# Performance work log

Measured on AMD Instinct MI355X. Metric: run time of the kernel, lower is better.

Reference implementation:

```python
import jax, jax.numpy as jnp
import numpy as np

B, L, HS = 32, 128, 512
P, M = 12, 1024
V, D = 50000, 128
P_TOTAL = 16
CHAR_LEN, CHAR_V = 16, 100
PRI_POS = (0, 1, 2, 3)  # privacy POS tags
TEMP = 1.0              # eval-mode temperature


def setup_inputs() -> dict:
    key = jax.random.key(0)
    ks = jax.random.split(key, 16)
    return {
        "ctx": jax.random.normal(ks[0], (B, L, HS), jnp.float32),
        "dec_W": jax.random.normal(ks[1], (P, HS, M), jnp.float32) * 0.05,
        "dec_b": jax.random.normal(ks[2], (P, M), jnp.float32) * 0.05,
        "psr_weight": jax.random.normal(ks[3], (V, D), jnp.float32),
        "atk_weight": jax.random.normal(ks[4], (V, D), jnp.float32),
        "cpy_W1": jax.random.normal(ks[5], (HS, 64), jnp.float32) * 0.05,
        "cpy_b1": jax.random.normal(ks[6], (64,), jnp.float32) * 0.05,
        "cpy_W2": jax.random.normal(ks[7], (64, 2), jnp.float32) * 0.05,
        "cpy_b2": jax.random.normal(ks[8], (2,), jnp.float32) * 0.05,
        "inp_word": jax.random.randint(ks[9], (B, L), 0, V),
        "inp_pos": jax.random.randint(ks[10], (B, L), 0, P_TOTAL),
        "inp_mask": jnp.ones((B, L), jnp.int32),
        "words": jax.random.randint(ks[11], (P, M), 0, V),
        "lut": jax.random.randint(ks[12], (V, CHAR_LEN), 0, CHAR_V),
    }


def _gumbel_softmax_hard(logits, key, t):
    # hard (straight-through) gumbel-softmax; forward value is one-hot
    u = jax.random.uniform(key, logits.shape, logits.dtype, 1e-6, 1.0 - 1e-6)
    g = -jnp.log(-jnp.log(u))
    y = jax.nn.softmax((logits + g) / t, axis=-1)
    idx = jnp.argmax(y, axis=-1)
    y_hard = jax.nn.one_hot(idx, logits.shape[-1], dtype=y.dtype)
    return y_hard + y - jax.lax.stop_gradient(y), idx


def reference(ctx, dec_W, dec_b, psr_weight, atk_weight,
              cpy_W1, cpy_b1, cpy_W2, cpy_b2,
              inp_word, inp_pos, inp_mask, words, lut):
    bs, ls = inp_word.shape
    N = bs * ls
    gkey = jax.random.key(42)

    ctx_f = ctx.reshape(N, -1)                      # [N, HS]
    pos_f = inp_pos.reshape(N)
    word_f = inp_word.reshape(N)

    ori_psr = psr_weight[word_f]                    # [N, D] gather
    ori_atk = atk_weight[word_f]
    obf_word = word_f
    obf_psr = ori_psr
    obf_atk = ori_atk
    obf_mask = jnp.zeros((N,), bool)
    pri_mask = jnp.zeros((N,), bool)
    entropy = jnp.float32(0.0)

    for p in range(P):  # small fixed set of POS tags (structurally distinct decoders)
        m = pos_f == p                              # [N] routing mask
        obf_mask = obf_mask | m
        if p in PRI_POS:
            pri_mask = pri_mask | m
        cnt = jnp.sum(m.astype(jnp.int32))
        logp = jax.nn.log_softmax(ctx_f @ dec_W[p] + dec_b[p], axis=-1)  # [N, M]
        ent_elem = -logp * jnp.exp(logp)
        ent_p = jnp.sum(jnp.where(m[:, None], ent_elem, 0.0)) / jnp.maximum(cnt * M, 1).astype(jnp.float32)
        entropy = entropy + jnp.where(cnt > 0, ent_p, 0.0)
        spt, idx = _gumbel_softmax_hard(logp, jax.random.fold_in(gkey, p), TEMP)
        spt_word = words[p][idx]                    # map local id -> vocab id
        obf_word = jnp.where(m, spt_word, obf_word)
        psr_p = spt @ psr_weight[words[p]]          # [N, D], per-POS sub-table
        atk_p = spt @ atk_weight[words[p]]
        obf_psr = jnp.where(m[:, None], psr_p, obf_psr)
        obf_atk = jnp.where(m[:, None], atk_p, obf_atk)

    # copy classifier
    h = jax.nn.relu(ctx_f @ cpy_W1 + cpy_b1)
    pcpy = jax.nn.log_softmax(h @ cpy_W2 + cpy_b2, axis=-1)  # [N, 2]
    # do_not_copy_pri: force pcpy to [0, 1] on privacy tokens
    pcpy = jnp.where(pri_mask[:, None], jnp.array([0.0, 1.0], pcpy.dtype), pcpy)

    cpy, _ = _gumbel_softmax_hard(pcpy, jax.random.fold_in(gkey, 999), TEMP)  # [N, 2]
    mask_f = inp_mask.reshape(N).astype(bool)
    cpy_mask = (cpy[:, 0] == 1.0) & mask_f

    noroot = inp_mask.astype(bool).at[:, 0].set(False).reshape(N)
    nr_cnt = jnp.maximum(jnp.sum(noroot.astype(jnp.int32)), 1).astype(jnp.float32)
    logp2 = jax.nn.log_softmax(pcpy, axis=-1)       # F.cross_entropy applies log_softmax again
    cpy_loss = -jnp.sum(jnp.where(noroot, logp2[:, 1], 0.0)) / nr_cnt  # cpy_penalty = 1.0 (applied twice)

    # use_copy: blend original vs obfuscated via (hard) copy gate
    c0, c1 = cpy[:, 0:1], cpy[:, 1:2]
    psr_out = (ori_psr * c0 + obf_psr * c1).reshape(bs, ls, -1)
    atk_out = (ori_atk * c0 + obf_atk * c1).reshape(bs, ls, -1)
    obf_mask = obf_mask & ~cpy_mask
    out_word = (word_f.astype(jnp.float32) * cpy[:, 0]
                + obf_word.astype(jnp.float32) * cpy[:, 1]).astype(jnp.int32).reshape(bs, ls)

    obf_char = lut[out_word]                        # [B, L, CHAR_LEN]
    ent_loss = -entropy  # ent_penalty = 1.0

    return (out_word, obf_char, psr_out, atk_out,
            obf_mask.reshape(bs, ls), cpy_mask.reshape(bs, ls),
            pri_mask.reshape(bs, ls), cpy_loss, ent_loss)
```

## Files before the change

### kernel.cpp

```cpp
#include <hip/hip_runtime.h>
#include <math.h>

#define BB 32
#define LL 128
#define HSZ 512
#define PP 12
#define MM 1024
#define VV 50000
#define DD 128
#define CLEN 16
#define NTOT 4096
#define LISTCAP 512

#define RT 64
#define CT 64
#define BK2 32
#define CPB 16

#define OFF_WORD  0
#define OFF_CHAR  4096
#define OFF_PSR   69632
#define OFF_ATK   593920
#define OFF_OBFM  1118208
#define OFF_CPYM  1122304
#define OFF_PRIM  1126400
#define OFF_CLOSS 1130496
#define OFF_ELOSS 1130497

#define WS_SC_OFF     6656
#define WS_LOGITS_OFF 16384

__device__ __forceinline__ float EXP32(float x){ return (float)exp((double)x); }
__device__ __forceinline__ float LOG32(float x){ return (float)log((double)x); }

__device__ __forceinline__ unsigned rotl32(unsigned x, int r){ return (x<<r)|(x>>(32-r)); }
__device__ __forceinline__ void tf2x32(unsigned k0, unsigned k1, unsigned x0, unsigned x1,
                                       unsigned &o0, unsigned &o1){
  unsigned ks2 = k0 ^ k1 ^ 0x1BD11BDAu;
  x0 += k0; x1 += k1;
  x0+=x1; x1=rotl32(x1,13); x1^=x0;
  x0+=x1; x1=rotl32(x1,15); x1^=x0;
  x0+=x1; x1=rotl32(x1,26); x1^=x0;
  x0+=x1; x1=rotl32(x1, 6); x1^=x0;
  x0+=k1; x1+=ks2+1u;
  x0+=x1; x1=rotl32(x1,17); x1^=x0;
  x0+=x1; x1=rotl32(x1,29); x1^=x0;
  x0+=x1; x1=rotl32(x1,16); x1^=x0;
  x0+=x1; x1=rotl32(x1,24); x1^=x0;
  x0+=ks2; x1+=k0+2u;
  x0+=x1; x1=rotl32(x1,13); x1^=x0;
  x0+=x1; x1=rotl32(x1,15); x1^=x0;
  x0+=x1; x1=rotl32(x1,26); x1^=x0;
  x0+=x1; x1=rotl32(x1, 6); x1^=x0;
  x0+=k0; x1+=k1+3u;
  x0+=x1; x1=rotl32(x1,17); x1^=x0;
  x0+=x1; x1=rotl32(x1,29); x1^=x0;
  x0+=x1; x1=rotl32(x1,16); x1^=x0;
  x0+=x1; x1=rotl32(x1,24); x1^=x0;
  x0+=k1; x1+=ks2+4u;
  x0+=x1; x1=rotl32(x1,13); x1^=x0;
  x0+=x1; x1=rotl32(x1,15); x1^=x0;
  x0+=x1; x1=rotl32(x1,26); x1^=x0;
  x0+=x1; x1=rotl32(x1, 6); x1^=x0;
  x0+=ks2; x1+=k0+5u;
  o0=x0; o1=x1;
}

__device__ __forceinline__ unsigned tf_bits32(unsigned k0, unsigned k1, unsigned e){
  unsigned o0, o1; tf2x32(k0, k1, 0u, e, o0, o1); return o0 ^ o1;
}

__device__ __forceinline__ float bits_to_unif(unsigned bits){
  const float lo = 1e-6f;
  const float hi = (float)(1.0 - 1e-6);
  const float span = hi - lo;
  unsigned fb = (bits >> 9) | 0x3f800000u;
  float f = __fsub_rn(__uint_as_float(fb), 1.0f);
  float r = __fadd_rn(__fmul_rn(f, span), lo);
  return fmaxf(lo, r);
}

__device__ __forceinline__ float gumbel_exact(unsigned bits){
  float u = bits_to_unif(bits);
  float v = -LOG32(u);
  return -LOG32(v);
}
__device__ __forceinline__ float gumbel_fast(unsigned bits){
  float u = bits_to_unif(bits);
  float v = -logf(u);
  return -logf(v);
}

__device__ __forceinline__ void gate_chain(int n, int pos,
                                           float p0f, float p1f,
                                           const float* __restrict__ cb2,
                                           float* __restrict__ sc_enc,
                                           float* __restrict__ l21_out)
{
  const bool ispri = (pos < 4);
  float pc0 = __fadd_rn(p0f, cb2[0]);
  float pc1 = __fadd_rn(p1f, cb2[1]);
  float m2  = fmaxf(pc0, pc1);
  float s0  = __fsub_rn(pc0, m2), s1 = __fsub_rn(pc1, m2);
  float se  = __fadd_rn(EXP32(s0), EXP32(s1));
  float lse = LOG32(se);
  float q0  = __fsub_rn(s0, lse), q1 = __fsub_rn(s1, lse);
  if (ispri){ q0 = 0.0f; q1 = 1.0f; }

  unsigned k90, k91; tf2x32(0u, 42u, 0u, 999u, k90, k91);
  float g0 = gumbel_exact(tf_bits32(k90, k91, (unsigned)(2*n)));
  float g1 = gumbel_exact(tf_bits32(k90, k91, (unsigned)(2*n + 1)));

  float x0 = __fadd_rn(q0, g0), x1 = __fadd_rn(q1, g1);
  float mmv = fmaxf(x0, x1);
  float ex0 = EXP32(__fsub_rn(x0, mmv));
  float ex1 = EXP32(__fsub_rn(x1, mmv));
  float ssum = __fadd_rn(ex0, ex1);
  float y0 = __fdiv_rn(ex0, ssum), y1 = __fdiv_rn(ex1, ssum);
  int   idx2 = (y1 > y0) ? 1 : 0;
  float ysel = idx2 ? y1 : y0;
  float c    = __fsub_rn(__fadd_rn(1.0f, ysel), ysel);
  *sc_enc = idx2 ? c : -c;

  float m3 = fmaxf(q0, q1);
  float t0 = __fsub_rn(q0, m3), t1 = __fsub_rn(q1, m3);
  float se2 = __fadd_rn(EXP32(t0), EXP32(t1));
  *l21_out = __fsub_rn(t1, LOG32(se2));
}

__global__ __launch_bounds__(256)
void bucket_kernel(const int* __restrict__ inp_pos, int* __restrict__ cntg,
                   int* __restrict__ rowlist)
{
  const int p = blockIdx.x;
  const int t = threadIdx.x;
  const int w = t >> 6, lane = t & 63;
  __shared__ int wtot[4];
  __shared__ int base_s;
  if (t == 0) base_s = 0;
  __syncthreads();
  for (int n0 = 0; n0 < NTOT; n0 += 256){
    int n = n0 + t;
    int m = (inp_pos[n] == p) ? 1 : 0;
    unsigned long long bal = __ballot(m);
    int excl = __popcll(bal & ((1ULL << lane) - 1ULL));
    if (lane == 0) wtot[w] = __popcll(bal);
    __syncthreads();
    int wbase = 0;
    #pragma unroll
    for (int i = 0; i < 4; ++i) if (i < w) wbase += wtot[i];
    int tot = wtot[0] + wtot[1] + wtot[2] + wtot[3];
    int b = base_s;
    if (m){
      int slot = b + wbase + excl;
      if (slot < LISTCAP) rowlist[p*LISTCAP + slot] = n;
    }
    __syncthreads();
    if (t == 0) base_s = b + tot;
    __syncthreads();
  }
  if (t == 0) cntg[p] = base_s;
}

__global__ __launch_bounds__(256)
void cpy_build_kernel(const float* __restrict__ ctx, const float* __restrict__ cW1,
                      const float* __restrict__ cb1, const float* __restrict__ cW2,
                      const float* __restrict__ cb2, const int* __restrict__ inp_pos,
                      float* __restrict__ scbuf)
{
  const int n0 = blockIdx.x * CPB;
  const int t = threadIdx.x;

  __shared__ float W1s[64][68];
  __shared__ float Cs[CPB][68];

  const int r  = t >> 4;
  const int og = (t & 15) * 4;
  double acc[4] = {0.0, 0.0, 0.0, 0.0};

  for (int k0 = 0; k0 < HSZ; k0 += 64){
    #pragma unroll
    for (int i = 0; i < 4; ++i){
      int s = t + i*256;
      int kk = s >> 4, q = s & 15;
      float4 v = *(const float4*)(cW1 + (size_t)(k0+kk)*64 + q*4);
      *(float4*)&W1s[kk][q*4] = v;
    }
    {
      int rr = t >> 4, q = t & 15;
      float4 v = *(const float4*)(ctx + (size_t)(n0+rr)*HSZ + k0 + q*4);
      *(float4*)&Cs[rr][q*4] = v;
    }
    __syncthreads();
    #pragma unroll 4
    for (int kk = 0; kk < 64; ++kk){
      double c = (double)Cs[r][kk];
      acc[0] += c * (double)W1s[kk][og+0];
      acc[1] += c * (double)W1s[kk][og+1];
      acc[2] += c * (double)W1s[kk][og+2];
      acc[3] += c * (double)W1s[kk][og+3];
    }
    __syncthreads();
  }

  double p0 = 0.0, p1 = 0.0;
  #pragma unroll
  for (int j = 0; j < 4; ++j){
    float hv = __fadd_rn((float)acc[j], cb1[og+j]);
    hv = hv > 0.f ? hv : 0.f;
    double hd = (double)hv;
    p0 += hd * (double)cW2[2*(og+j)+0];
    p1 += hd * (double)cW2[2*(og+j)+1];
  }
  #pragma unroll
  for (int off = 1; off < 16; off <<= 1){
    p0 += __shfl_xor(p0, off);
    p1 += __shfl_xor(p1, off);
  }

  if ((t & 15) == 0){
    const int n = n0 + r;
    float senc, l21;
    gate_chain(n, inp_pos[n], (float)p0, (float)p1, cb2, &senc, &l21);
    scbuf[2*n + 0] = senc;
    scbuf[2*n + 1] = l21;
  }
}

__global__ __launch_bounds__(256)
void gemm_kernel(const float* __restrict__ ctx, const float* __restrict__ dec_W,
                 const int* __restrict__ cntg, const int* __restrict__ rowlist,
                 float* __restrict__ logits)
{
  const int p  = blockIdx.z;
  const int c0 = blockIdx.x * CT;
  const int r0 = blockIdx.y * RT;
  const int cnt0 = cntg[p];
  const int cnt  = cnt0 < LISTCAP ? cnt0 : LISTCAP;
  if (r0 >= cnt) return;
  const int t = threadIdx.x;

  __shared__ double As[RT][BK2+2];
  __shared__ double Bs[BK2][16][6];
  __shared__ int    rid_s[RT];

  if (t < RT){
    int rr = r0 + t;
    rid_s[t] = rowlist[p*LISTCAP + (rr < cnt ? rr : cnt-1)];
  }
  __syncthreads();

  const int tr = t >> 4, tc = t & 15;
  double acc[4][4];
  #pragma unroll
  for (int i = 0; i < 4; ++i)
    #pragma unroll
    for (int j = 0; j < 4; ++j) acc[i][j] = 0.0;

  const float* Wp = dec_W + (size_t)p * HSZ * MM;

  for (int k0 = 0; k0 < HSZ; k0 += BK2){
    #pragma unroll
    for (int i = 0; i < 2; ++i){
      int s = t + i*256;
      int rr = s >> 3, q = s & 7;
      float4 v = *(const float4*)(ctx + (size_t)rid_s[rr]*HSZ + k0 + q*4);
      double2 d0; d0.x = (double)v.x; d0.y = (double)v.y;
      double2 d1; d1.x = (double)v.z; d1.y = (double)v.w;
      *(double2*)&As[rr][q*4 + 0] = d0;
      *(double2*)&As[rr][q*4 + 2] = d1;
    }
    #pragma unroll
    for (int i = 0; i < 2; ++i){
      int s = t + i*256;
      int kk = s >> 4, q = s & 15;
      float4 v = *(const float4*)(Wp + (size_t)(k0+kk)*MM + c0 + q*4);
      double2 d0; d0.x = (double)v.x; d0.y = (double)v.y;
      double2 d1; d1.x = (double)v.z; d1.y = (double)v.w;
      *(double2*)&Bs[kk][q][0] = d0;
      *(double2*)&Bs[kk][q][2] = d1;
    }
    __syncthreads();
    #pragma unroll 4
    for (int kk = 0; kk < BK2; ++kk){
      double b0 = Bs[kk][tc][0];
      double b1 = Bs[kk][tc][1];
      double b2 = Bs[kk][tc][2];
      double b3 = Bs[kk][tc][3];
      double a0 = As[tr*4+0][kk];
      double a1 = As[tr*4+1][kk];
      double a2 = As[tr*4+2][kk];
      double a3 = As[tr*4+3][kk];
      acc[0][0]+=a0*b0; acc[0][1]+=a0*b1; acc[0][2]+=a0*b2; acc[0][3]+=a0*b3;
      acc[1][0]+=a1*b0; acc[1][1]+=a1*b1; acc[1][2]+=a1*b2; acc[1][3]+=a1*b3;
      acc[2][0]+=a2*b0; acc[2][1]+=a2*b1; acc[2][2]+=a2*b2; acc[2][3]+=a2*b3;
      acc[3][0]+=a3*b0; acc[3][1]+=a3*b1; acc[3][2]+=a3*b2; acc[3][3]+=a3*b3;
    }
    __syncthreads();
  }

  #pragma unroll
  for (int i = 0; i < 4; ++i){
    int rr = r0 + tr*4 + i;
    if (rr < cnt){
      int rg = rid_s[tr*4 + i];
      float4 o;
      o.x=(float)acc[i][0]; o.y=(float)acc[i][1]; o.z=(float)acc[i][2]; o.w=(float)acc[i][3];
      *(float4*)(logits + (size_t)rg*MM + c0 + tc*4) = o;
    }
  }
}

__global__ __launch_bounds__(256)
void finalize_kernel(const float* __restrict__ dec_b,
                     const float* __restrict__ psr_w, const float* __restrict__ atk_w,
                     const int* __restrict__ inp_word, const int* __restrict__ inp_pos,
                     const int* __restrict__ inp_mask, const int* __restrict__ words,
                     const int* __restrict__ lut, float* __restrict__ logitsbuf,
                     const float* __restrict__ scbuf,
                     float* __restrict__ out)
{
  const int wid = threadIdx.x >> 6, lane = threadIdx.x & 63;
  const int n = blockIdx.x * 4 + wid;

  const int  pos   = inp_pos[n];
  const int  word  = inp_word[n];
  const int  msk   = inp_mask[n];
  const bool isobf = (pos < PP);
  const bool ispri = (pos < 4);
  const float senc = scbuf[2*n + 0];
  const float c0 = (senc < 0.f) ? -senc : 0.f;
  const float c1 = (senc < 0.f) ? 0.f : senc;

  int bi = 0;
  if (isobf){
    float l[16];
    float lm = -3.4e38f;
    #pragma unroll
    for (int it = 0; it < 4; ++it){
      int m = it*256 + lane*4;
      float4 lg = *(const float4*)(logitsbuf + (size_t)n*MM + m);
      float4 bq = *(const float4*)(dec_b + (size_t)pos*MM + m);
      l[it*4+0] = __fadd_rn(lg.x, bq.x);
      l[it*4+1] = __fadd_rn(lg.y, bq.y);
      l[it*4+2] = __fadd_rn(lg.z, bq.z);
      l[it*4+3] = __fadd_rn(lg.w, bq.w);
      lm = fmaxf(lm, fmaxf(fmaxf(l[it*4+0], l[it*4+1]), fmaxf(l[it*4+2], l[it*4+3])));
    }
    #pragma unroll
    for (int off = 32; off > 0; off >>= 1) lm = fmaxf(lm, __shfl_xor(lm, off));
    const float xmax = lm;

    float e[16];
    double ds = 0.0;
    #pragma unroll
    for (int j = 0; j < 16; ++j){
      e[j] = expf(__fsub_rn(l[j], xmax));
      ds += (double)e[j];
    }
    #pragma unroll
    for (int off = 32; off > 0; off >>= 1) ds += __shfl_xor(ds, off);
    const double se = ds;
    const float lse = logf((float)se);
    const double inv_se = 1.0 / se;

    unsigned kp0, kp1; tf2x32(0u, 42u, 0u, (unsigned)pos, kp0, kp1);
    float best = -3.4e38f; double es = 0.0;
    #pragma unroll
    for (int it = 0; it < 4; ++it){
      #pragma unroll
      for (int j = 0; j < 4; ++j){
        int m = it*256 + lane*4 + j;
        float sh = __fsub_rn(l[it*4+j], xmax);
        float lp = __fsub_rn(sh, lse);
        es += (double)(-lp) * ((double)e[it*4+j] * inv_se);
        float g = gumbel_fast(tf_bits32(kp0, kp1, (unsigned)(n*MM + m)));
        float sv = __fadd_rn(lp, g);
        if (sv > best){ best = sv; bi = m; }
      }
    }
    #pragma unroll
    for (int off = 32; off > 0; off >>= 1){
      float ov = __shfl_xor(best, off);
      int   oi = __shfl_xor(bi,   off);
      if (ov > best || (ov == best && oi < bi)){ best = ov; bi = oi; }
      es += __shfl_xor(es, off);
    }
    if (lane == 0) logitsbuf[(size_t)n*MM] = (float)es;
  } else {
    if (lane == 0) logitsbuf[(size_t)n*MM] = 0.f;
  }

  const int obf_word = isobf ? words[pos*MM + bi] : word;
  float of = __fadd_rn(__fmul_rn((float)word, c0), __fmul_rn((float)obf_word, c1));
  int ow = (int)of;
  if (lane == 0){
    out[OFF_WORD + n] = (float)ow;
    bool cpym = (c0 == 1.0f) && (msk != 0);
    out[OFF_CPYM + n] = cpym ? 1.f : 0.f;
    out[OFF_OBFM + n] = (isobf && !cpym) ? 1.f : 0.f;
    out[OFF_PRIM + n] = ispri ? 1.f : 0.f;
  }
  if (lane < CLEN)
    out[OFF_CHAR + (size_t)n*CLEN + lane] = (float)lut[(size_t)ow*CLEN + lane];
  #pragma unroll
  for (int rep = 0; rep < 2; ++rep){
    int j = lane + rep*64;
    float po = psr_w[(size_t)word*DD + j];
    float pb = isobf ? psr_w[(size_t)obf_word*DD + j] : po;
    out[OFF_PSR + (size_t)n*DD + j] = __fadd_rn(__fmul_rn(po, c0), __fmul_rn(pb, c1));
    float ao = atk_w[(size_t)word*DD + j];
    float ab = isobf ? atk_w[(size_t)obf_word*DD + j] : ao;
    out[OFF_ATK + (size_t)n*DD + j] = __fadd_rn(__fmul_rn(ao, c0), __fmul_rn(ab, c1));
  }
}

__global__ __launch_bounds__(1024)
void fin2_kernel(const int* __restrict__ inp_pos, const int* __restrict__ inp_mask,
                 const float* __restrict__ scbuf, const float* __restrict__ logitsbuf,
                 float* __restrict__ out)
{
  const int t = threadIdx.x;
  const int w = t >> 6, lane = t & 63;
  __shared__ double s_ent[PP];
  __shared__ int    s_cnt[PP];
  __shared__ double s_cl;
  __shared__ int    s_nr;

  if (w < PP){
    const int p = w;
    double es = 0.0; int c = 0;
    for (int n = lane; n < NTOT; n += 64){
      if (inp_pos[n] == p){
        es += (double)logitsbuf[(size_t)n*MM];
        c  += 1;
      }
    }
    #pragma unroll
    for (int off = 1; off < 64; off <<= 1){
      es += __shfl_xor(es, off);
      c  += __shfl_xor(c, off);
    }
    if (lane == 0){ s_ent[p] = es; s_cnt[p] = c; }
  } else if (w == PP){
    double cl = 0.0; int nr = 0;
    for (int n = lane; n < NTOT; n += 64){
      if (inp_mask[n] != 0 && (n & (LL-1)) != 0){
        cl += (double)scbuf[2*n + 1];
        nr += 1;
      }
    }
    #pragma unroll
    for (int off = 1; off < 64; off <<= 1){
      cl += __shfl_xor(cl, off);
      nr += __shfl_xor(nr, off);
    }
    if (lane == 0){ s_cl = cl; s_nr = nr; }
  }
  __syncthreads();
  if (t == 0){
    float ent = 0.f;
    for (int p = 0; p < PP; ++p){
      int c = s_cnt[p];
      if (c > 0){
        int denom = c * MM; if (denom < 1) denom = 1;
        ent = __fadd_rn(ent, __fdiv_rn((float)s_ent[p], (float)denom));
      }
    }
    out[OFF_ELOSS] = -ent;
    int nrc = s_nr; if (nrc < 1) nrc = 1;
    out[OFF_CLOSS] = -__fdiv_rn((float)s_cl, (float)nrc);
  }
}

__global__ __launch_bounds__(256)
void fin_kernel(const int* __restrict__ inp_pos, const int* __restrict__ inp_mask,
                const float* __restrict__ ws, float* __restrict__ out)
{
  __shared__ int cnt[PP];
  __shared__ int nr;
  int t = threadIdx.x;
  if (t < PP) cnt[t] = 0;
  if (t == 0) nr = 0;
  __syncthreads();
  int ln = 0;
  for (int n = t; n < NTOT; n += 256){
    int p = inp_pos[n];
    if (p < PP) atomicAdd(&cnt[p], 1);
    if (inp_mask[n] != 0 && (n & (LL-1)) != 0) ln++;
  }
  atomicAdd(&nr, ln);
  __syncthreads();
  if (t == 0){
    float ent = 0.f;
    for (int p = 0; p < PP; ++p){
      int c = cnt[p];
      if (c > 0){
        int denom = c * MM; if (denom < 1) denom = 1;
        ent = __fadd_rn(ent, __fdiv_rn(ws[p], (float)denom));
      }
    }
    out[OFF_ELOSS] = -ent;
    int nrc = nr; if (nrc < 1) nrc = 1;
    out[OFF_CLOSS] = -__fdiv_rn(ws[12], (float)nrc);
  }
}

__global__ __launch_bounds__(256)
void row_kernel_mono(const float* __restrict__ ctx, const float* __restrict__ dec_W,
                const float* __restrict__ dec_b, const float* __restrict__ psr_w,
                const float* __restrict__ atk_w, const float* __restrict__ cW1,
                const float* __restrict__ cb1, const float* __restrict__ cW2,
                const float* __restrict__ cb2, const int* __restrict__ inp_word,
                const int* __restrict__ inp_pos, const int* __restrict__ inp_mask,
                const int* __restrict__ words, const int* __restrict__ lut,
                float* __restrict__ out, float* __restrict__ ws)
{
  const int n = blockIdx.x;
  const int t = threadIdx.x;

  __shared__ float  ctx_s[HSZ];
  __shared__ float  logit_s[MM];
  __shared__ float  h_s[64];
  __shared__ double redd[256];
  __shared__ float  redf[256];
  __shared__ int    redi[256];
  __shared__ float  sc[2];
  __shared__ int    si[1];

  for (int k = t; k < HSZ; k += 256) ctx_s[k] = ctx[(size_t)n*HSZ + k];
  __syncthreads();

  const int  pos   = inp_pos[n];
  const int  word  = inp_word[n];
  const int  msk   = inp_mask[n];
  const bool isobf = (pos < PP);
  const bool ispri = (pos < 4);

  if (t < 64){
    double acc = 0.0;
    for (int k = 0; k < HSZ; ++k) acc += (double)ctx_s[k] * (double)cW1[k*64 + t];
    float hv = __fadd_rn((float)acc, cb1[t]);
    h_s[t] = hv > 0.f ? hv : 0.f;
  }
  __syncthreads();

  if (t == 0){
    double a0 = 0.0, a1 = 0.0;
    for (int k = 0; k < 64; ++k){
      double hv = (double)h_s[k];
      a0 += hv * (double)cW2[k*2 + 0];
      a1 += hv * (double)cW2[k*2 + 1];
    }
    float senc, l21;
    gate_chain(n, pos, (float)a0, (float)a1, cb2, &senc, &l21);
    sc[0] = (senc < 0.f) ? -senc : 0.f;
    sc[1] = (senc < 0.f) ? 0.f : senc;
    if (msk != 0 && (n & (LL-1)) != 0) atomicAdd(ws + 12, l21);
  }

  if (isobf){
    const float4* W4 = (const float4*)(dec_W + (size_t)pos * HSZ * MM);
    double a0=0.0, a1=0.0, a2=0.0, a3=0.0;
    for (int k = 0; k < HSZ; ++k){
      double c = (double)ctx_s[k];
      float4 w = W4[(size_t)k*256 + t];
      a0 += c*(double)w.x; a1 += c*(double)w.y; a2 += c*(double)w.z; a3 += c*(double)w.w;
    }
    const float* bp = dec_b + (size_t)pos * MM;
    const int m0 = 4*t;
    logit_s[m0+0] = __fadd_rn((float)a0, bp[m0+0]);
    logit_s[m0+1] = __fadd_rn((float)a1, bp[m0+1]);
    logit_s[m0+2] = __fadd_rn((float)a2, bp[m0+2]);
    logit_s[m0+3] = __fadd_rn((float)a3, bp[m0+3]);
    __syncthreads();

    float lm = logit_s[m0];
    lm = fmaxf(lm, logit_s[m0+1]); lm = fmaxf(lm, logit_s[m0+2]); lm = fmaxf(lm, logit_s[m0+3]);
    redf[t] = lm; __syncthreads();
    for (int s = 128; s > 0; s >>= 1){ if (t < s) redf[t] = fmaxf(redf[t], redf[t+s]); __syncthreads(); }
    const float xmax = redf[0];
    __syncthreads();

    double dsm = 0.0;
    for (int j = 0; j < 4; ++j)
      dsm += (double)EXP32(__fsub_rn(logit_s[m0+j], xmax));
    redd[t] = dsm; __syncthreads();
    for (int s = 128; s > 0; s >>= 1){ if (t < s) redd[t] += redd[t+s]; __syncthreads(); }
    const float lse = LOG32((float)redd[0]);
    __syncthreads();

    unsigned kp0, kp1; tf2x32(0u, 42u, 0u, (unsigned)pos, kp0, kp1);
    float best = -3.4e38f; int bi = 0; double es = 0.0;
    for (int j = 0; j < 4; ++j){
      int m = m0 + j;
      float sh = __fsub_rn(logit_s[m], xmax);
      float lp = __fsub_rn(sh, lse);
      float ex = EXP32(lp);
      es += (double)__fmul_rn(-lp, ex);
      float g = gumbel_exact(tf_bits32(kp0, kp1, (unsigned)(n*MM + m)));
      float sv = __fadd_rn(lp, g);
      if (sv > best){ best = sv; bi = m; }
    }
    redf[t] = best; redi[t] = bi; redd[t] = es; __syncthreads();
    for (int s = 128; s > 0; s >>= 1){
      if (t < s){
        float v2 = redf[t+s]; int i2 = redi[t+s];
        if (v2 > redf[t] || (v2 == redf[t] && i2 < redi[t])){ redf[t] = v2; redi[t] = i2; }
        redd[t] += redd[t+s];
      }
      __syncthreads();
    }
    if (t == 0){ si[0] = redi[0]; atomicAdd(ws + pos, (float)redd[0]); }
    __syncthreads();
  } else {
    __syncthreads();
  }

  const int   idx = isobf ? si[0] : 0;
  const float c0 = sc[0], c1 = sc[1];
  const int   obf_word = isobf ? words[pos*MM + idx] : word;

  if (t == 0){
    float of = __fadd_rn(__fmul_rn((float)word, c0), __fmul_rn((float)obf_word, c1));
    int ow = (int)of;
    out[OFF_WORD + n] = (float)ow;
    bool cpym = (c0 == 1.0f) && (msk != 0);
    out[OFF_CPYM + n] = cpym ? 1.f : 0.f;
    out[OFF_OBFM + n] = (isobf && !cpym) ? 1.f : 0.f;
    out[OFF_PRIM + n] = ispri ? 1.f : 0.f;
    #pragma unroll
    for (int j = 0; j < CLEN; ++j)
      out[OFF_CHAR + (size_t)n*CLEN + j] = (float)lut[(size_t)ow*CLEN + j];
  }
  if (t < DD){
    float po = psr_w[(size_t)word*DD + t];
    float pb = isobf ? psr_w[(size_t)obf_word*DD + t] : po;
    out[OFF_PSR + (size_t)n*DD + t] = __fadd_rn(__fmul_rn(po, c0), __fmul_rn(pb, c1));
    float ao = atk_w[(size_t)word*DD + t];
    float ab = isobf ? atk_w[(size_t)obf_word*DD + t] : ao;
    out[OFF_ATK + (size_t)n*DD + t] = __fadd_rn(__fmul_rn(ao, c0), __fmul_rn(ab, c1));
  }
}

extern "C" void kernel_launch(void* const* d_in, const int* in_sizes, int n_in,
                              void* d_out, int out_size, void* d_ws, size_t ws_size,
                              hipStream_t stream)
{
  const float* ctx      = (const float*)d_in[0];
  const float* dec_W    = (const float*)d_in[1];
  const float* dec_b    = (const float*)d_in[2];
  const float* psr_w    = (const float*)d_in[3];
  const float* atk_w    = (const float*)d_in[4];
  const float* cW1      = (const float*)d_in[5];
  const float* cb1      = (const float*)d_in[6];
  const float* cW2      = (const float*)d_in[7];
  const float* cb2      = (const float*)d_in[8];
  const int*   inp_word = (const int*)d_in[9];
  const int*   inp_pos  = (const int*)d_in[10];
  const int*   inp_mask = (const int*)d_in[11];
  const int*   words    = (const int*)d_in[12];
  const int*   lut      = (const int*)d_in[13];
  float* out = (float*)d_out;
  float* ws  = (float*)d_ws;

  const size_t need = ((size_t)WS_LOGITS_OFF + (size_t)NTOT*MM) * 4;

  if (ws_size >= need){
    int*   cntg      = (int*)ws + 16;
    int*   rowlist   = (int*)ws + 64;
    float* scbuf     = ws + WS_SC_OFF;
    float* logitsbuf = ws + WS_LOGITS_OFF;
    bucket_kernel<<<PP, 256, 0, stream>>>(inp_pos, cntg, rowlist);
    cpy_build_kernel<<<NTOT/CPB, 256, 0, stream>>>(ctx, cW1, cb1, cW2, cb2,
                                                   inp_pos, scbuf);
    gemm_kernel<<<dim3(MM/CT, LISTCAP/RT, PP), 256, 0, stream>>>(ctx, dec_W, cntg,
                                                                 rowlist, logitsbuf);
    finalize_kernel<<<NTOT/4, 256, 0, stream>>>(dec_b, psr_w, atk_w,
                                                inp_word, inp_pos, inp_mask, words, lut,
                                                logitsbuf, scbuf, out);
    fin2_kernel<<<1, 1024, 0, stream>>>(inp_pos, inp_mask, scbuf, logitsbuf, out);
  } else {
    hipMemsetAsync(ws, 0, 512, stream);
    row_kernel_mono<<<NTOT, 256, 0, stream>>>(ctx, dec_W, dec_b, psr_w, atk_w,
                                              cW1, cb1, cW2, cb2,
                                              inp_word, inp_pos, inp_mask, words, lut,
                                              out, ws);
    fin_kernel<<<1, 256, 0, stream>>>(inp_pos, inp_mask, ws, out);
  }
}
```

Before: 322.6 us.

## Merge bucket into cpy_build and fold final reduction into finalize via last-block

The row-bucketing work moves into extra blocks of the cpy_build launch, and the single-block loss reduction runs in whichever finalize block finishes last, tracked by an atomic counter. This removes two kernel launches and their serialization gaps, at the cost of a memset and a last-block tail that runs on only four waves instead of sixteen. The inner cpy loop also now reads W1 as one float4 instead of four scalar loads.

```diff
diff --git a/kernel.cpp b/kernel.cpp
--- a/kernel.cpp
+++ b/kernel.cpp
@@ -16,6 +16,7 @@
 #define CT 64
 #define BK2 32
 #define CPB 16
+#define NCPB (NTOT/CPB)
 
 #define OFF_WORD  0
 #define OFF_CHAR  4096
@@ -129,47 +130,46 @@
 }
 
 __global__ __launch_bounds__(256)
-void bucket_kernel(const int* __restrict__ inp_pos, int* __restrict__ cntg,
-                   int* __restrict__ rowlist)
-{
-  const int p = blockIdx.x;
-  const int t = threadIdx.x;
-  const int w = t >> 6, lane = t & 63;
-  __shared__ int wtot[4];
-  __shared__ int base_s;
-  if (t == 0) base_s = 0;
-  __syncthreads();
-  for (int n0 = 0; n0 < NTOT; n0 += 256){
-    int n = n0 + t;
-    int m = (inp_pos[n] == p) ? 1 : 0;
-    unsigned long long bal = __ballot(m);
-    int excl = __popcll(bal & ((1ULL << lane) - 1ULL));
-    if (lane == 0) wtot[w] = __popcll(bal);
-    __syncthreads();
-    int wbase = 0;
-    #pragma unroll
-    for (int i = 0; i < 4; ++i) if (i < w) wbase += wtot[i];
-    int tot = wtot[0] + wtot[1] + wtot[2] + wtot[3];
-    int b = base_s;
-    if (m){
-      int slot = b + wbase + excl;
-      if (slot < LISTCAP) rowlist[p*LISTCAP + slot] = n;
-    }
-    __syncthreads();
-    if (t == 0) base_s = b + tot;
-    __syncthreads();
-  }
-  if (t == 0) cntg[p] = base_s;
-}
-
-__global__ __launch_bounds__(256)
 void cpy_build_kernel(const float* __restrict__ ctx, const float* __restrict__ cW1,
                       const float* __restrict__ cb1, const float* __restrict__ cW2,
                       const float* __restrict__ cb2, const int* __restrict__ inp_pos,
+                      int* __restrict__ cntg, int* __restrict__ rowlist,
                       float* __restrict__ scbuf)
 {
+  const int t = threadIdx.x;
+
+  if (blockIdx.x >= NCPB){
+    const int p = blockIdx.x - NCPB;
+    const int w = t >> 6, lane = t & 63;
+    __shared__ int wtot[4];
+    __shared__ int base_s;
+    if (t == 0) base_s = 0;
+    __syncthreads();
+    for (int n0 = 0; n0 < NTOT; n0 += 256){
+      int n = n0 + t;
+      int m = (inp_pos[n] == p) ? 1 : 0;
+      unsigned long long bal = __ballot(m);
+      int excl = __popcll(bal & ((1ULL << lane) - 1ULL));
+      if (lane == 0) wtot[w] = __popcll(bal);
+      __syncthreads();
+      int wbase = 0;
+      #pragma unroll
+      for (int i = 0; i < 4; ++i) if (i < w) wbase += wtot[i];
+      int tot = wtot[0] + wtot[1] + wtot[2] + wtot[3];
+      int b = base_s;
+      if (m){
+        int slot = b + wbase + excl;
+        if (slot < LISTCAP) rowlist[p*LISTCAP + slot] = n;
+      }
+      __syncthreads();
+      if (t == 0) base_s = b + tot;
+      __syncthreads();
+    }
+    if (t == 0) cntg[p] = base_s;
+    return;
+  }
+
   const int n0 = blockIdx.x * CPB;
-  const int t = threadIdx.x;
 
   __shared__ float W1s[64][68];
   __shared__ float Cs[CPB][68];
@@ -194,11 +194,12 @@
     __syncthreads();
     #pragma unroll 4
     for (int kk = 0; kk < 64; ++kk){
+      float4 wv = *(const float4*)&W1s[kk][og];
       double c = (double)Cs[r][kk];
-      acc[0] += c * (double)W1s[kk][og+0];
-      acc[1] += c * (double)W1s[kk][og+1];
-      acc[2] += c * (double)W1s[kk][og+2];
-      acc[3] += c * (double)W1s[kk][og+3];
+      acc[0] += c * (double)wv.x;
+      acc[1] += c * (double)wv.y;
+      acc[2] += c * (double)wv.z;
+      acc[3] += c * (double)wv.w;
     }
     __syncthreads();
   }
@@ -317,7 +318,7 @@
                      const int* __restrict__ inp_word, const int* __restrict__ inp_pos,
                      const int* __restrict__ inp_mask, const int* __restrict__ words,
                      const int* __restrict__ lut, float* __restrict__ logitsbuf,
-                     const float* __restrict__ scbuf,
+                     const float* __restrict__ scbuf, int* __restrict__ done_cnt,
                      float* __restrict__ out)
 {
   const int wid = threadIdx.x >> 6, lane = threadIdx.x & 63;
@@ -413,63 +414,66 @@
     float ab = isobf ? atk_w[(size_t)obf_word*DD + j] : ao;
     out[OFF_ATK + (size_t)n*DD + j] = __fadd_rn(__fmul_rn(ao, c0), __fmul_rn(ab, c1));
   }
-}
-
-__global__ __launch_bounds__(1024)
-void fin2_kernel(const int* __restrict__ inp_pos, const int* __restrict__ inp_mask,
-                 const float* __restrict__ scbuf, const float* __restrict__ logitsbuf,
-                 float* __restrict__ out)
-{
-  const int t = threadIdx.x;
-  const int w = t >> 6, lane = t & 63;
+
+  __shared__ int is_last;
   __shared__ double s_ent[PP];
   __shared__ int    s_cnt[PP];
   __shared__ double s_cl;
   __shared__ int    s_nr;
-
-  if (w < PP){
-    const int p = w;
-    double es = 0.0; int c = 0;
-    for (int n = lane; n < NTOT; n += 64){
-      if (inp_pos[n] == p){
-        es += (double)logitsbuf[(size_t)n*MM];
-        c  += 1;
-      }
-    }
-    #pragma unroll
-    for (int off = 1; off < 64; off <<= 1){
-      es += __shfl_xor(es, off);
-      c  += __shfl_xor(c, off);
-    }
-    if (lane == 0){ s_ent[p] = es; s_cnt[p] = c; }
-  } else if (w == PP){
-    double cl = 0.0; int nr = 0;
-    for (int n = lane; n < NTOT; n += 64){
-      if (inp_mask[n] != 0 && (n & (LL-1)) != 0){
-        cl += (double)scbuf[2*n + 1];
-        nr += 1;
-      }
-    }
-    #pragma unroll
-    for (int off = 1; off < 64; off <<= 1){
-      cl += __shfl_xor(cl, off);
-      nr += __shfl_xor(nr, off);
-    }
-    if (lane == 0){ s_cl = cl; s_nr = nr; }
-  }
+  __threadfence();
   __syncthreads();
-  if (t == 0){
-    float ent = 0.f;
-    for (int p = 0; p < PP; ++p){
-      int c = s_cnt[p];
-      if (c > 0){
-        int denom = c * MM; if (denom < 1) denom = 1;
-        ent = __fadd_rn(ent, __fdiv_rn((float)s_ent[p], (float)denom));
-      }
-    }
-    out[OFF_ELOSS] = -ent;
-    int nrc = s_nr; if (nrc < 1) nrc = 1;
-    out[OFF_CLOSS] = -__fdiv_rn((float)s_cl, (float)nrc);
+  if (threadIdx.x == 0){
+    int d = atomicAdd(done_cnt, 1);
+    is_last = (d == (int)gridDim.x - 1) ? 1 : 0;
+  }
+  __syncthreads();
+  if (is_last){
+    __threadfence();
+    for (int j = 0; j < 3; ++j){
+      int p = wid + 4*j;
+      double es = 0.0; int c = 0;
+      for (int nn = lane; nn < NTOT; nn += 64){
+        if (inp_pos[nn] == p){
+          es += (double)logitsbuf[(size_t)nn*MM];
+          c  += 1;
+        }
+      }
+      #pragma unroll
+      for (int off = 1; off < 64; off <<= 1){
+        es += __shfl_xor(es, off);
+        c  += __shfl_xor(c, off);
+      }
+      if (lane == 0){ s_ent[p] = es; s_cnt[p] = c; }
+    }
+    if (wid == 0){
+      double cl = 0.0; int nr = 0;
+      for (int nn = lane; nn < NTOT; nn += 64){
+        if (inp_mask[nn] != 0 && (nn & (LL-1)) != 0){
+          cl += (double)scbuf[2*nn + 1];
+          nr += 1;
+        }
+      }
+      #pragma unroll
+      for (int off = 1; off < 64; off <<= 1){
+        cl += __shfl_xor(cl, off);
+        nr += __shfl_xor(nr, off);
+      }
+      if (lane == 0){ s_cl = cl; s_nr = nr; }
+    }
+    __syncthreads();
+    if (threadIdx.x == 0){
+      float ent = 0.f;
+      for (int p = 0; p < PP; ++p){
+        int c = s_cnt[p];
+        if (c > 0){
+          int denom = c * MM; if (denom < 1) denom = 1;
+          ent = __fadd_rn(ent, __fdiv_rn((float)s_ent[p], (float)denom));
+        }
+      }
+      out[OFF_ELOSS] = -ent;
+      int nrc = s_nr; if (nrc < 1) nrc = 1;
+      out[OFF_CLOSS] = -__fdiv_rn((float)s_cl, (float)nrc);
+    }
   }
 }
 
@@ -668,18 +672,18 @@
 
   if (ws_size >= need){
     int*   cntg      = (int*)ws + 16;
+    int*   done_cnt  = (int*)ws + 28;
     int*   rowlist   = (int*)ws + 64;
     float* scbuf     = ws + WS_SC_OFF;
     float* logitsbuf = ws + WS_LOGITS_OFF;
-    bucket_kernel<<<PP, 256, 0, stream>>>(inp_pos, cntg, rowlist);
-    cpy_build_kernel<<<NTOT/CPB, 256, 0, stream>>>(ctx, cW1, cb1, cW2, cb2,
-                                                   inp_pos, scbuf);
+    hipMemsetAsync(done_cnt, 0, 4, stream);
+    cpy_build_kernel<<<NCPB + PP, 256, 0, stream>>>(ctx, cW1, cb1, cW2, cb2,
+                                                    inp_pos, cntg, rowlist, scbuf);
     gemm_kernel<<<dim3(MM/CT, LISTCAP/RT, PP), 256, 0, stream>>>(ctx, dec_W, cntg,
                                                                  rowlist, logitsbuf);
     finalize_kernel<<<NTOT/4, 256, 0, stream>>>(dec_b, psr_w, atk_w,
                                                 inp_word, inp_pos, inp_mask, words, lut,
-                                                logitsbuf, scbuf, out);
-    fin2_kernel<<<1, 1024, 0, stream>>>(inp_pos, inp_mask, scbuf, logitsbuf, out);
+                                                logitsbuf, scbuf, done_cnt, out);
   } else {
     hipMemsetAsync(ws, 0, 512, stream);
     row_kernel_mono<<<NTOT, 256, 0, stream>>>(ctx, dec_W, dec_b, psr_w, atk_w,
```

After: 483.9 us. 50.0% more time.
